# Kernel tuning notes

Measured on AMD Instinct MI355X. Metric: run time of the kernel, lower is better.

The kernel has to match this reference:

```python
import jax, jax.numpy as jnp
import numpy as np

B, T, IN, H = 16, 1024, 1024, 1024


def setup_inputs() -> dict:
    key = jax.random.key(0)
    ks = jax.random.split(key, 6)
    s_in = 1.0 / np.sqrt(IN)
    s_out = 1.0 / np.sqrt(2 * H)
    return {
        "x": jax.random.normal(ks[0], (B, T, IN), jnp.float32),
        "W_in": jax.random.uniform(ks[1], (H, IN), jnp.float32, -s_in, s_in),
        "b_in": jax.random.uniform(ks[2], (H,), jnp.float32, -s_in, s_in),
        "leak_tau_v": jax.random.normal(ks[3], (H,), jnp.float32),
        "flip_threshold": jnp.full((H,), 0.5, jnp.float32),
        "W_out": jax.random.uniform(ks[4], (H, 2 * H), jnp.float32, -s_out, s_out),
        "b_out": jax.random.uniform(ks[5], (H,), jnp.float32, -s_out, s_out),
    }


def _hsru_scan(I_tbh, alpha, thr):
    """Leaky-integrate / threshold-reset recurrence over time.
    I_tbh: [T,B,H]; alpha, thr: [H]. Returns (v_seq, spike_seq) each [T,B,H].
    v_t = alpha*v_{t-1} + I_t; spike on crossing threshold; v reset on spike.
    """
    def step(v, I_t):
        v = alpha * v + I_t
        spike = (v > thr).astype(v.dtype)  # hard threshold; zero grad (as in torch)
        v = v * (1.0 - spike)              # reset membrane on flip
        return v, (v, spike)

    v0 = jnp.zeros(I_tbh.shape[1:], I_tbh.dtype)
    _, (v_seq, s_seq) = jax.lax.scan(step, v0, I_tbh)
    return v_seq, s_seq


def reference(x, W_in, b_in, leak_tau_v, flip_threshold, W_out, b_out):
    # input currents: [B,T,H]
    I = jnp.einsum('bti,hi->bth', x, W_in) + b_in
    alpha = jnp.exp(-jax.nn.softplus(leak_tau_v))  # [H], in (0,1)
    v_seq, s_seq = _hsru_scan(jnp.swapaxes(I, 0, 1), alpha, flip_threshold)
    combined = jnp.concatenate([v_seq, s_seq], axis=-1)   # [T,B,2H]
    combined = jnp.swapaxes(combined, 0, 1)               # [B,T,2H]
    return jnp.tanh(jnp.einsum('btk,hk->bth', combined, W_out) + b_out)
```

## Files before the change

kernel.cpp:

```cpp
#include <hip/hip_runtime.h>
#include <hip/hip_bf16.h>
#include <cmath>


typedef __attribute__((ext_vector_type(8))) __bf16 bf16x8;
typedef __attribute__((ext_vector_type(4))) __bf16 bf16x4;
typedef __attribute__((ext_vector_type(4))) float  f32x4;

#define LDT 40
#define LDF 36

__global__ __launch_bounds__(256)
void gemm1_f32chain_kernel(const float* __restrict__ X,
                           const float* __restrict__ W,
                           const float* __restrict__ bias,
                           float* __restrict__ I)
{
    __shared__ __align__(16) float sA[128][LDF];
    __shared__ __align__(16) float sB[128][LDF];

    const int tid  = threadIdx.x;
    const int bn   = blockIdx.x;
    const int bm   = blockIdx.y;
    const int row0 = bm * 128;
    const int col0 = bn * 128;
    const int tx   = tid & 15;
    const int ty   = tid >> 4;

    float acc[8][8];
    #pragma unroll
    for (int i = 0; i < 8; ++i)
        #pragma unroll
        for (int j = 0; j < 8; ++j)
            acc[i][j] = 0.0f;

    for (int k0 = 0; k0 < 1024; k0 += 32) {
        #pragma unroll
        for (int i = 0; i < 4; ++i) {
            int q  = tid + i * 256;
            int r  = q >> 3;
            int c4 = (q & 7) * 4;
            *(f32x4*)&sA[r][c4] = *(const f32x4*)&X[(size_t)(row0 + r) * 1024 + k0 + c4];
            *(f32x4*)&sB[r][c4] = *(const f32x4*)&W[(size_t)(col0 + r) * 1024 + k0 + c4];
        }
        __syncthreads();

        #pragma unroll
        for (int kk = 0; kk < 32; kk += 4) {
            f32x4 a4[8], b4[8];
            #pragma unroll
            for (int i = 0; i < 8; ++i) a4[i] = *(const f32x4*)&sA[ty + 16 * i][kk];
            #pragma unroll
            for (int j = 0; j < 8; ++j) b4[j] = *(const f32x4*)&sB[tx + 16 * j][kk];
            #pragma unroll
            for (int q = 0; q < 4; ++q)
                #pragma unroll
                for (int i = 0; i < 8; ++i)
                    #pragma unroll
                    for (int j = 0; j < 8; ++j)
                        acc[i][j] = fmaf(a4[i][q], b4[j][q], acc[i][j]);
        }
        __syncthreads();
    }

    #pragma unroll
    for (int i = 0; i < 8; ++i)
        #pragma unroll
        for (int j = 0; j < 8; ++j) {
            int rg = row0 + ty + 16 * i;
            int cg = col0 + tx + 16 * j;
            I[(size_t)rg * 1024 + cg] = __fadd_rn(acc[i][j], bias[cg]);
        }
}

__global__ __launch_bounds__(64)
void hsru_scan_f32_kernel(const float* __restrict__ I,
                          const float* __restrict__ leak,
                          const float* __restrict__ thr,
                          __bf16* __restrict__ comb)
{
    int g = blockIdx.x * 64 + threadIdx.x;
    int b = g >> 10;
    int h = g & 1023;

    float lt = leak[h];
    float e     = (float)exp(-(double)fabsf(lt));
    float l1    = (float)log1p((double)e);
    float sp    = __fadd_rn(fmaxf(lt, 0.0f), l1);
    float alpha = (float)exp(-(double)sp);
    float th    = thr[h];

    const float* Ip = I    + (size_t)b * (1024 * 1024) + h;
    __bf16*      cp = comb + (size_t)b * (1024 * 2048) + h;

    float buf[16], nxt[16];
    #pragma unroll
    for (int j = 0; j < 16; ++j) buf[j] = Ip[(size_t)j * 1024];

    float v = 0.0f;
    for (int t0 = 0; t0 < 1024; t0 += 16) {
        if (t0 + 16 < 1024) {
            #pragma unroll
            for (int j = 0; j < 16; ++j)
                nxt[j] = Ip[(size_t)(t0 + 16 + j) * 1024];
        }
        #pragma unroll
        for (int j = 0; j < 16; ++j) {
            float cur = buf[j];
            v = __fadd_rn(__fmul_rn(alpha, v), cur);
            float spike = (v > th) ? 1.0f : 0.0f;
            v = __fmul_rn(v, __fsub_rn(1.0f, spike));
            cp[(size_t)(t0 + j) * 2048]        = (__bf16)v;
            cp[(size_t)(t0 + j) * 2048 + 1024] = (__bf16)spike;
        }
        if (t0 + 16 < 1024) {
            #pragma unroll
            for (int j = 0; j < 16; ++j) buf[j] = nxt[j];
        }
    }
}

__global__ __launch_bounds__(256)
void wcvt_kernel(const float* __restrict__ W, __bf16* __restrict__ Wb)
{
    int idx = (blockIdx.x * 256 + threadIdx.x) * 8;
    f32x4 v0 = *(const f32x4*)&W[idx];
    f32x4 v1 = *(const f32x4*)&W[idx + 4];
    bf16x8 o;
    #pragma unroll
    for (int j = 0; j < 4; ++j) { o[j] = (__bf16)v0[j]; o[4 + j] = (__bf16)v1[j]; }
    *(bf16x8*)&Wb[idx] = o;
}

__global__ __launch_bounds__(256)
void gemm2_kernel(const __bf16* __restrict__ A,
                  const __bf16* __restrict__ Wb,
                  const float* __restrict__ bias,
                  float* __restrict__ O)
{
    __shared__ __align__(16) __bf16 sA[128][LDT];
    __shared__ __align__(16) __bf16 sB[128][LDT];

    const int tid  = threadIdx.x;
    const int bn   = blockIdx.x;
    const int bm   = blockIdx.y;
    const int row0 = bm * 128;
    const int col0 = bn * 128;

    const int lane = tid & 63;
    const int wid  = tid >> 6;
    const int wm   = (wid >> 1) * 64;
    const int wn   = (wid & 1) * 64;

    f32x4 acc[4][4];
    #pragma unroll
    for (int i = 0; i < 4; ++i)
        #pragma unroll
        for (int j = 0; j < 4; ++j)
            acc[i][j] = f32x4{0.f, 0.f, 0.f, 0.f};

    const int frow  = lane & 15;
    const int fkoff = (lane >> 4) * 8;

    for (int k0 = 0; k0 < 2048; k0 += 32) {
        #pragma unroll
        for (int i = 0; i < 2; ++i) {
            int q  = tid + i * 256;
            int r  = q >> 2;
            int c8 = (q & 3) * 8;
            *(bf16x8*)&sA[r][c8] = *(const bf16x8*)&A [(size_t)(row0 + r) * 2048 + k0 + c8];
            *(bf16x8*)&sB[r][c8] = *(const bf16x8*)&Wb[(size_t)(col0 + r) * 2048 + k0 + c8];
        }
        __syncthreads();

        bf16x8 a_f[4], b_f[4];
        #pragma unroll
        for (int f = 0; f < 4; ++f) {
            a_f[f] = *(const bf16x8*)&sA[wm + f * 16 + frow][fkoff];
            b_f[f] = *(const bf16x8*)&sB[wn + f * 16 + frow][fkoff];
        }
        #pragma unroll
        for (int fm = 0; fm < 4; ++fm)
            #pragma unroll
            for (int fn = 0; fn < 4; ++fn)
                acc[fm][fn] = __builtin_amdgcn_mfma_f32_16x16x32_bf16(a_f[fm], b_f[fn], acc[fm][fn], 0, 0, 0);
        __syncthreads();
    }

    const int crow = (lane >> 4) * 4;
    const int ccol = lane & 15;
    #pragma unroll
    for (int fm = 0; fm < 4; ++fm)
        #pragma unroll
        for (int fn = 0; fn < 4; ++fn)
            #pragma unroll
            for (int j = 0; j < 4; ++j) {
                int rg = row0 + wm + fm * 16 + crow + j;
                int cg = col0 + wn + fn * 16 + ccol;
                O[(size_t)rg * 1024 + cg] = tanhf(acc[fm][fn][j] + bias[cg]);
            }
}

extern "C" void kernel_launch(void* const* d_in, const int* in_sizes, int n_in,
                              void* d_out, int out_size, void* d_ws, size_t ws_size,
                              hipStream_t stream)
{
    const float* x     = (const float*)d_in[0];
    const float* W_in  = (const float*)d_in[1];
    const float* b_in  = (const float*)d_in[2];
    const float* leak  = (const float*)d_in[3];
    const float* thr   = (const float*)d_in[4];
    const float* W_out = (const float*)d_in[5];
    const float* b_out = (const float*)d_in[6];

    const size_t NEED = (64ull << 20) + (4ull << 20);
    if (ws_size < NEED) return;

    float*  out  = (float*)d_out;
    __bf16* comb = (__bf16*)d_ws;
    __bf16* Wb   = (__bf16*)((char*)d_ws + (64ull << 20));

    dim3 grid(8, 128);

    wcvt_kernel<<<1024, 256, 0, stream>>>(W_out, Wb);
    gemm1_f32chain_kernel<<<grid, 256, 0, stream>>>(x, W_in, b_in, out);
    hsru_scan_f32_kernel<<<256, 64, 0, stream>>>(out, leak, thr, comb);
    gemm2_kernel<<<grid, 256, 0, stream>>>(comb, Wb, b_out, out);
}
```

Baseline: 576.1 us.

## Restructure fp32 input GEMM to one row per thread with broadcast weight loads

The first GEMM now has each thread own one row of a 256-row tile across 32 output columns. Only X is staged in LDS, and the weights are read directly from global memory at wave-uniform addresses, so they can become scalar broadcast loads. This cuts LDS reads per FMA sharply and keeps the sequential fp32 k-order accumulation. The cost is that X is re-fetched for every 32-column block, which quadruples X traffic through L2. The tile is written out through LDS so the global stores stay coalesced.

```diff
diff --git a/kernel.cpp b/kernel.cpp
--- a/kernel.cpp
+++ b/kernel.cpp
@@ -8,7 +8,7 @@
 typedef __attribute__((ext_vector_type(4))) float  f32x4;
 
 #define LDT 40
-#define LDF 36
+#define LDA1 36
 
 __global__ __launch_bounds__(256)
 void gemm1_f32chain_kernel(const float* __restrict__ X,
@@ -16,61 +16,61 @@
                            const float* __restrict__ bias,
                            float* __restrict__ I)
 {
-    __shared__ __align__(16) float sA[128][LDF];
-    __shared__ __align__(16) float sB[128][LDF];
+    __shared__ __align__(16) float sA[256][LDA1];
 
     const int tid  = threadIdx.x;
     const int bn   = blockIdx.x;
     const int bm   = blockIdx.y;
-    const int row0 = bm * 128;
-    const int col0 = bn * 128;
-    const int tx   = tid & 15;
-    const int ty   = tid >> 4;
-
-    float acc[8][8];
-    #pragma unroll
-    for (int i = 0; i < 8; ++i)
-        #pragma unroll
-        for (int j = 0; j < 8; ++j)
-            acc[i][j] = 0.0f;
+    const int row0 = bm * 256;
+    const int col0 = bn * 32;
+    const int w    = tid >> 6;
+    const int l    = tid & 63;
+    const int myrow = w * 64 + l;
+
+    float acc[32];
+    #pragma unroll
+    for (int j = 0; j < 32; ++j) acc[j] = 0.0f;
 
     for (int k0 = 0; k0 < 1024; k0 += 32) {
         #pragma unroll
-        for (int i = 0; i < 4; ++i) {
+        for (int i = 0; i < 8; ++i) {
             int q  = tid + i * 256;
             int r  = q >> 3;
             int c4 = (q & 7) * 4;
             *(f32x4*)&sA[r][c4] = *(const f32x4*)&X[(size_t)(row0 + r) * 1024 + k0 + c4];
-            *(f32x4*)&sB[r][c4] = *(const f32x4*)&W[(size_t)(col0 + r) * 1024 + k0 + c4];
         }
         __syncthreads();
 
         #pragma unroll
         for (int kk = 0; kk < 32; kk += 4) {
-            f32x4 a4[8], b4[8];
-            #pragma unroll
-            for (int i = 0; i < 8; ++i) a4[i] = *(const f32x4*)&sA[ty + 16 * i][kk];
-            #pragma unroll
-            for (int j = 0; j < 8; ++j) b4[j] = *(const f32x4*)&sB[tx + 16 * j][kk];
-            #pragma unroll
-            for (int q = 0; q < 4; ++q)
+            const f32x4 a4 = *(const f32x4*)&sA[myrow][kk];
+            #pragma unroll
+            for (int j = 0; j < 32; ++j) {
+                const float* wp = &W[(size_t)(col0 + j) * 1024 + k0 + kk];
                 #pragma unroll
-                for (int i = 0; i < 8; ++i)
-                    #pragma unroll
-                    for (int j = 0; j < 8; ++j)
-                        acc[i][j] = fmaf(a4[i][q], b4[j][q], acc[i][j]);
-        }
-        __syncthreads();
-    }
-
-    #pragma unroll
-    for (int i = 0; i < 8; ++i)
-        #pragma unroll
-        for (int j = 0; j < 8; ++j) {
-            int rg = row0 + ty + 16 * i;
-            int cg = col0 + tx + 16 * j;
-            I[(size_t)rg * 1024 + cg] = __fadd_rn(acc[i][j], bias[cg]);
-        }
+                for (int q = 0; q < 4; ++q)
+                    acc[j] = fmaf(a4[q], wp[q], acc[j]);
+            }
+        }
+        __syncthreads();
+    }
+
+    #pragma unroll
+    for (int j = 0; j < 32; ++j)
+        acc[j] = __fadd_rn(acc[j], bias[col0 + j]);
+
+    #pragma unroll
+    for (int j = 0; j < 32; ++j)
+        sA[w * 64 + l][j] = acc[j];
+
+    const int jc = l & 31;
+    const int rh = l >> 5;
+    #pragma unroll
+    for (int s = 0; s < 32; ++s) {
+        int rl = 2 * s + rh;
+        float val = sA[w * 64 + rl][jc];
+        I[(size_t)(row0 + w * 64 + rl) * 1024 + col0 + jc] = val;
+    }
 }
 
 __global__ __launch_bounds__(64)
@@ -220,10 +220,8 @@
     __bf16* comb = (__bf16*)d_ws;
     __bf16* Wb   = (__bf16*)((char*)d_ws + (64ull << 20));
 
-    dim3 grid(8, 128);
-
     wcvt_kernel<<<1024, 256, 0, stream>>>(W_out, Wb);
-    gemm1_f32chain_kernel<<<grid, 256, 0, stream>>>(x, W_in, b_in, out);
+    gemm1_f32chain_kernel<<<dim3(32, 64), 256, 0, stream>>>(x, W_in, b_in, out);
     hsru_scan_f32_kernel<<<256, 64, 0, stream>>>(out, leak, thr, comb);
-    gemm2_kernel<<<grid, 256, 0, stream>>>(comb, Wb, b_out, out);
-}
+    gemm2_kernel<<<dim3(8, 128), 256, 0, stream>>>(comb, Wb, b_out, out);
+}
```

After: 1.521 ms. +164.0%, slower.
